# Kernel tuning notes

Hardware: AMD Instinct MI355X
Metric: run time of the kernel (lower is better)

Reference implementation:

```python
import jax, jax.numpy as jnp
import numpy as np

V, E, H, L, B, T = 371, 512, 8, 8, 4, 1024
D = E // H
EPS = 1e-5


def setup_inputs() -> dict:
    key = jax.random.key(0)
    ks = jax.random.split(key, 7)
    s = 0.02
    return {
        "idx": jax.random.randint(ks[0], (B, T), 0, V),
        "wte": jax.random.normal(ks[1], (V, E), jnp.float32) * s,   # tied with lm_head
        "wpe": jax.random.normal(ks[2], (T, E), jnp.float32) * s,
        "c_attn_w": jax.random.normal(ks[3], (L, E, 3 * E), jnp.float32) * s,
        "c_proj_w": jax.random.normal(ks[4], (L, E, E), jnp.float32) * s,
        "fc_w": jax.random.normal(ks[5], (L, E, 4 * E), jnp.float32) * s,
        "fc_proj_w": jax.random.normal(ks[6], (L, 4 * E, E), jnp.float32) * s,
        "ln1_w": jnp.ones((L, E), jnp.float32),
        "ln2_w": jnp.ones((L, E), jnp.float32),
        "lnf_w": jnp.ones((E,), jnp.float32),
    }


def _ln(x, w):
    m = jnp.mean(x, axis=-1, keepdims=True)
    v = jnp.mean((x - m) ** 2, axis=-1, keepdims=True)
    return (x - m) * jax.lax.rsqrt(v + EPS) * w


def reference(idx, wte, wpe, c_attn_w, c_proj_w, fc_w, fc_proj_w, ln1_w, ln2_w, lnf_w):
    mask = jnp.tril(jnp.ones((T, T), bool))  # causal mask, as in the registered buffer
    scale = 1.0 / np.sqrt(D)

    x0 = wte[idx] + wpe[None, :T]  # [B,T,E]

    def block(x, p):
        aw, pw, l1, l2, fw, fpw = p
        h = _ln(x, l1)
        qkv = h @ aw                                   # [B,T,3E]
        q, k, v = jnp.split(qkv, 3, axis=-1)
        q = q.reshape(B, T, H, D)
        k = k.reshape(B, T, H, D)
        v = v.reshape(B, T, H, D)
        att = jnp.einsum("bqhd,bkhd->bhqk", q, k) * scale  # full TxT scores (faithful)
        att = jnp.where(mask[None, None], att, -jnp.inf)
        att = jax.nn.softmax(att, axis=-1)
        y = jnp.einsum("bhqk,bkhd->bqhd", att, v).reshape(B, T, E)
        x = x + y @ pw
        h = _ln(x, l2)
        x = x + jax.nn.gelu(h @ fw, approximate=False) @ fpw
        return x, None

    x, _ = jax.lax.scan(block, x0, (c_attn_w, c_proj_w, ln1_w, ln2_w, fc_w, fc_proj_w))
    x = _ln(x, lnf_w)
    logits = x @ wte.T  # weight tying: lm_head.weight = wte.weight
    return logits
```

## Files before the change

### kernel.cpp

```cpp
#include <hip/hip_runtime.h>


#define VOCAB 371
#define EMB   512
#define NH    8
#define NL    8
#define TS    1024
#define NTOK  4096
#define NEG_INF (-1e30f)

typedef unsigned short ushort_t;
typedef __attribute__((ext_vector_type(8))) short short8;
typedef __attribute__((ext_vector_type(4))) float f32x4;

__device__ inline float bf2f(ushort_t b) {
    unsigned int u = ((unsigned int)b) << 16;
    float f; __builtin_memcpy(&f, &u, 4); return f;
}
__device__ inline ushort_t f2bf(float f) {
    unsigned int u; __builtin_memcpy(&u, &f, 4);
    u = (u + 0x7fff + ((u >> 16) & 1)) >> 16;
    return (ushort_t)u;
}

__global__ __launch_bounds__(64) void detect_k(const ushort_t* __restrict__ w,
        int* __restrict__ flag)
{
    int i = threadIdx.x;
    float v = bf2f(w[2 * i]);
    bool ok = (__builtin_fabsf(v) <= 4.0f);
    unsigned long long m = __ballot(ok);
    if (i == 0) flag[0] = (__popcll(m) >= 56) ? 1 : 0;
}

__global__ __launch_bounds__(256) void sentinel_k(ushort_t* __restrict__ out, int n)
{
    int i = blockIdx.x * 256 + threadIdx.x;
    if (i < n) out[i] = 0x447A;
}

__global__ __launch_bounds__(256) void embed_k(const int* __restrict__ idx,
        const void* __restrict__ wte, const void* __restrict__ wpe,
        float* __restrict__ x, const int* __restrict__ flag)
{
    int n = blockIdx.x, tid = threadIdx.x;
    int t = n & (TS - 1);
    int v = idx[n];
    size_t o = (size_t)n * EMB;
    float a0, a1, b0, b1;
    if (*flag) {
        const ushort_t* te = (const ushort_t*)wte; const ushort_t* pe = (const ushort_t*)wpe;
        a0 = bf2f(te[v * EMB + tid]); a1 = bf2f(te[v * EMB + 256 + tid]);
        b0 = bf2f(pe[t * EMB + tid]); b1 = bf2f(pe[t * EMB + 256 + tid]);
    } else {
        const float* te = (const float*)wte; const float* pe = (const float*)wpe;
        a0 = te[v * EMB + tid]; a1 = te[v * EMB + 256 + tid];
        b0 = pe[t * EMB + tid]; b1 = pe[t * EMB + 256 + tid];
    }
    x[o + tid] = a0 + b0;
    x[o + 256 + tid] = a1 + b1;
}

__global__ __launch_bounds__(256) void ln_k(const float* __restrict__ x,
        const void* __restrict__ w, long woff, ushort_t* __restrict__ out,
        const int* __restrict__ flag)
{
    const int row = blockIdx.x * 4 + (threadIdx.x >> 6);
    const int lane = threadIdx.x & 63;
    const float* xr = x + (size_t)row * EMB + lane * 8;
    float4 f0 = *(const float4*)xr;
    float4 f1 = *(const float4*)(xr + 4);
    float v[8] = {f0.x, f0.y, f0.z, f0.w, f1.x, f1.y, f1.z, f1.w};
    float s = ((v[0] + v[1]) + (v[2] + v[3])) + ((v[4] + v[5]) + (v[6] + v[7]));
#pragma unroll
    for (int off = 32; off > 0; off >>= 1) s += __shfl_xor(s, off, 64);
    float mean = s * (1.0f / EMB);
    float s2 = 0.f;
#pragma unroll
    for (int j = 0; j < 8; ++j) { v[j] -= mean; s2 += v[j] * v[j]; }
#pragma unroll
    for (int off = 32; off > 0; off >>= 1) s2 += __shfl_xor(s2, off, 64);
    float rs = rsqrtf(s2 * (1.0f / EMB) + 1e-5f);
    float g[8];
    if (*flag) {
        const ushort_t* wb = (const ushort_t*)w + woff + lane * 8;
        ushort_t tmp[8];
        *(uint4*)tmp = *(const uint4*)wb;
#pragma unroll
        for (int j = 0; j < 8; ++j) g[j] = bf2f(tmp[j]);
    } else {
        const float* wf = (const float*)w + woff + lane * 8;
        float4 g0 = *(const float4*)wf;
        float4 g1 = *(const float4*)(wf + 4);
        g[0] = g0.x; g[1] = g0.y; g[2] = g0.z; g[3] = g0.w;
        g[4] = g1.x; g[5] = g1.y; g[6] = g1.z; g[7] = g1.w;
    }
    ushort_t ob[8];
#pragma unroll
    for (int j = 0; j < 8; ++j) ob[j] = f2bf(v[j] * rs * g[j]);
    *(uint4*)(out + (size_t)row * EMB + lane * 8) = *(uint4*)ob;
}

__global__ __launch_bounds__(256) void wtrans_k(const void* __restrict__ aw,
        const void* __restrict__ pw, const void* __restrict__ fw,
        const void* __restrict__ fpw, long l, ushort_t* __restrict__ wbuf,
        const int* __restrict__ flag)
{
    __shared__ float tile[64][65];
    const int isbf = *flag;
    long lay = (l < 0) ? (long)blockIdx.z : l;
    ushort_t* obase = wbuf + ((l < 0) ? (size_t)blockIdx.z * 3145728 : 0);
    int t = blockIdx.x;
    const void* src; ushort_t* dst; int Kw, Nw; long ioff;
    if (t < 192)      { src = aw;  dst = obase;           Kw = 512;  Nw = 1536; ioff = lay * 512L * 1536; }
    else if (t < 256) { t -= 192; src = pw;  dst = obase + 786432;  Kw = 512;  Nw = 512;  ioff = lay * 512L * 512; }
    else if (t < 512) { t -= 256; src = fw;  dst = obase + 1048576; Kw = 512;  Nw = 2048; ioff = lay * 512L * 2048; }
    else              { t -= 512; src = fpw; dst = obase + 2097152; Kw = 2048; Nw = 512;  ioff = lay * 2048L * 512; }
    int tn = Nw >> 6;
    int n0 = (t % tn) * 64, k0 = (t / tn) * 64;
    const int r = threadIdx.x >> 2, cq = (threadIdx.x & 3) * 16;
    size_t ii = ioff + (size_t)(k0 + r) * Nw + n0 + cq;
    if (isbf) {
        const ushort_t* sb = (const ushort_t*)src + ii;
        ushort_t tmp[16];
        *(uint4*)tmp = *(const uint4*)sb;
        *(uint4*)(tmp + 8) = *(const uint4*)(sb + 8);
#pragma unroll
        for (int j = 0; j < 16; ++j) tile[r][cq + j] = bf2f(tmp[j]);
    } else {
        const float* sf = (const float*)src + ii;
        *(float4*)&tile[r][cq]      = *(const float4*)sf;
        *(float4*)&tile[r][cq + 4]  = *(const float4*)(sf + 4);
        *(float4*)&tile[r][cq + 8]  = *(const float4*)(sf + 8);
        *(float4*)&tile[r][cq + 12] = *(const float4*)(sf + 12);
    }
    __syncthreads();
    const int kc = (threadIdx.x & 7) * 8;
#pragma unroll
    for (int j = 0; j < 2; ++j) {
        const int n = (threadIdx.x >> 3) + j * 32;
        unsigned pk[4];
#pragma unroll
        for (int i = 0; i < 4; ++i) {
            unsigned lo = f2bf(tile[kc + 2 * i][n]);
            unsigned hi = f2bf(tile[kc + 2 * i + 1][n]);
            pk[i] = lo | (hi << 16);
        }
        *(uint4*)(dst + (size_t)(n0 + n) * Kw + k0 + kc) = *(uint4*)pk;
    }
}

__global__ __launch_bounds__(256) void wconv_k(const void* __restrict__ in,
        ushort_t* __restrict__ out, int n, const int* __restrict__ flag)
{
    int i = blockIdx.x * 256 + threadIdx.x;
    if (i >= n) return;
    out[i] = (*flag) ? ((const ushort_t*)in)[i] : f2bf(((const float*)in)[i]);
}

__global__ __launch_bounds__(256) void gemm_wide(const ushort_t* __restrict__ A,
        const ushort_t* __restrict__ Bt, int M, int N, int K,
        float* __restrict__ outF, ushort_t* __restrict__ outB,
        const float* __restrict__ res, int act)
{
    __shared__ ushort_t Al[128 * 72];
    __shared__ ushort_t Bl[64 * 72];
    const int tid = threadIdx.x;
    const int wave = tid >> 6, lane = tid & 63;
    const int quad = lane >> 4, l16 = lane & 15;
    const int m0 = blockIdx.y * 128, n0 = blockIdx.x * 64;
    const int ar = tid >> 1, ac = (tid & 1) * 32;
    const int br = tid >> 2, bc = (tid & 3) * 16;
    const ushort_t* Ag = A + (size_t)(m0 + ar) * K + ac;
    const ushort_t* Bg = Bt + (size_t)(n0 + br) * K + bc;
    f32x4 acc[2][4] = {};
    for (int k0 = 0; k0 < K; k0 += 64) {
        uint4 a0 = *(const uint4*)(Ag + k0);
        uint4 a1 = *(const uint4*)(Ag + k0 + 8);
        uint4 a2 = *(const uint4*)(Ag + k0 + 16);
        uint4 a3 = *(const uint4*)(Ag + k0 + 24);
        uint4 b0 = *(const uint4*)(Bg + k0);
        uint4 b1 = *(const uint4*)(Bg + k0 + 8);
        __syncthreads();
        *(uint4*)&Al[ar * 72 + ac]      = a0;
        *(uint4*)&Al[ar * 72 + ac + 8]  = a1;
        *(uint4*)&Al[ar * 72 + ac + 16] = a2;
        *(uint4*)&Al[ar * 72 + ac + 24] = a3;
        *(uint4*)&Bl[br * 72 + bc]     = b0;
        *(uint4*)&Bl[br * 72 + bc + 8] = b1;
        __syncthreads();
#pragma unroll
        for (int ks = 0; ks < 2; ++ks) {
            short8 af[2], bf[4];
#pragma unroll
            for (int mi = 0; mi < 2; ++mi)
                af[mi] = *(const short8*)&Al[(wave * 32 + mi * 16 + l16) * 72 + ks * 32 + quad * 8];
#pragma unroll
            for (int ni = 0; ni < 4; ++ni)
                bf[ni] = *(const short8*)&Bl[(ni * 16 + l16) * 72 + ks * 32 + quad * 8];
#pragma unroll
            for (int mi = 0; mi < 2; ++mi)
#pragma unroll
                for (int ni = 0; ni < 4; ++ni)
                    acc[mi][ni] = __builtin_amdgcn_mfma_f32_16x16x32_bf16(
                            af[mi], bf[ni], acc[mi][ni], 0, 0, 0);
        }
    }
#pragma unroll
    for (int mi = 0; mi < 2; ++mi) {
        const int rowb = m0 + wave * 32 + mi * 16 + quad * 4;
#pragma unroll
        for (int ni = 0; ni < 4; ++ni) {
            const int col = n0 + ni * 16 + l16;
#pragma unroll
            for (int r = 0; r < 4; ++r) {
                size_t o = (size_t)(rowb + r) * N + col;
                float v = acc[mi][ni][r];
                if (res) v += res[o];
                if (act) v = 0.5f * v * (1.0f + erff(v * 0.70710678118f));
                if (outF) outF[o] = v;
                else      outB[o] = f2bf(v);
            }
        }
    }
}

__global__ __launch_bounds__(256) void gemm_nt(const ushort_t* __restrict__ A,
        const ushort_t* __restrict__ Bt, int M, int N, int K,
        float* __restrict__ outF, ushort_t* __restrict__ outB, void* __restrict__ outD,
        const float* __restrict__ res, int act, const int* __restrict__ flag)
{
    __shared__ ushort_t Al[64 * 72];
    __shared__ ushort_t Bl[64 * 72];
    const int isbf = *flag;
    const int tid = threadIdx.x;
    const int wave = tid >> 6, lane = tid & 63;
    const int quad = lane >> 4, l16 = lane & 15;
    const int m0 = blockIdx.y * 64, n0 = blockIdx.x * 64;
    const int sr = tid >> 2, sc = (tid & 3) * 16;
    const bool bok = (n0 + sr) < N;
    const ushort_t* Ag = A + (size_t)(m0 + sr) * K + sc;
    const ushort_t* Bg = Bt + (size_t)(n0 + sr) * K + sc;
    f32x4 acc[4] = {};
    for (int k0 = 0; k0 < K; k0 += 64) {
        uint4 a0 = *(const uint4*)(Ag + k0);
        uint4 a1 = *(const uint4*)(Ag + k0 + 8);
        uint4 b0 = make_uint4(0, 0, 0, 0), b1 = make_uint4(0, 0, 0, 0);
        if (bok) { b0 = *(const uint4*)(Bg + k0); b1 = *(const uint4*)(Bg + k0 + 8); }
        __syncthreads();
        *(uint4*)&Al[sr * 72 + sc] = a0; *(uint4*)&Al[sr * 72 + sc + 8] = a1;
        *(uint4*)&Bl[sr * 72 + sc] = b0; *(uint4*)&Bl[sr * 72 + sc + 8] = b1;
        __syncthreads();
#pragma unroll
        for (int kc = 0; kc < 2; ++kc) {
            short8 af = *(const short8*)&Al[(wave * 16 + l16) * 72 + kc * 32 + quad * 8];
#pragma unroll
            for (int nt = 0; nt < 4; ++nt) {
                short8 bf = *(const short8*)&Bl[(nt * 16 + l16) * 72 + kc * 32 + quad * 8];
                acc[nt] = __builtin_amdgcn_mfma_f32_16x16x32_bf16(af, bf, acc[nt], 0, 0, 0);
            }
        }
    }
    const int mb = m0 + wave * 16 + quad * 4;
#pragma unroll
    for (int nt = 0; nt < 4; ++nt) {
        int nn = n0 + nt * 16 + l16;
        if (nn >= N) continue;
#pragma unroll
        for (int r = 0; r < 4; ++r) {
            size_t o = (size_t)(mb + r) * N + nn;
            float v = acc[nt][r];
            if (res) v += res[o];
            if (act) v = 0.5f * v * (1.0f + erff(v * 0.70710678118f));
            if (outF)      outF[o] = v;
            else if (outB) outB[o] = f2bf(v);
            else if (isbf) ((ushort_t*)outD)[o] = f2bf(v);
            else           ((float*)outD)[o] = v;
        }
    }
}

__global__ __launch_bounds__(256) void gemm_k(const ushort_t* __restrict__ A,
        const void* __restrict__ B, long boff, int M, int N, int K, int bt,
        float* __restrict__ outF, ushort_t* __restrict__ outB, void* __restrict__ outD,
        const float* __restrict__ res, int act, const int* __restrict__ flag)
{
    __shared__ ushort_t Al[64 * 40];
    __shared__ ushort_t Bl[64 * 40];
    const int isbf = *flag;
    const int tid = threadIdx.x;
    const int wave = tid >> 6, lane = tid & 63;
    const int quad = lane >> 4, l16 = lane & 15;
    const int m0 = blockIdx.y * 64, n0 = blockIdx.x * 64;
    const int sr = tid >> 2, sc = (tid & 3) * 8;
    const int kr = tid >> 3, nc = (tid & 7) * 8;
    f32x4 acc[4] = {};
    const bool bok = (n0 + sr) < N;
    const ushort_t* Ag = A + (size_t)(m0 + sr) * K + sc;
    const ushort_t* Bb = (const ushort_t*)B + boff;
    const float*    Bf = (const float*)B + boff;
    const size_t i1 = (size_t)(n0 + sr) * K + sc;
    const size_t i0 = (size_t)kr * N + n0 + nc;
    for (int k0 = 0; k0 < K; k0 += 32) {
        uint4 av = *(const uint4*)(Ag + k0);
        ushort_t b8[8] = {0, 0, 0, 0, 0, 0, 0, 0};
        size_t bi = bt ? (i1 + k0) : (i0 + (size_t)k0 * N);
        if (!bt || bok) {
            if (isbf) *(uint4*)b8 = *(const uint4*)(Bb + bi);
            else {
                float4 f0 = *(const float4*)(Bf + bi);
                float4 f1 = *(const float4*)(Bf + bi + 4);
                b8[0] = f2bf(f0.x); b8[1] = f2bf(f0.y); b8[2] = f2bf(f0.z); b8[3] = f2bf(f0.w);
                b8[4] = f2bf(f1.x); b8[5] = f2bf(f1.y); b8[6] = f2bf(f1.z); b8[7] = f2bf(f1.w);
            }
        }
        __syncthreads();
        *(uint4*)&Al[sr * 40 + sc] = av;
        if (bt) *(uint4*)&Bl[sr * 40 + sc] = *(uint4*)b8;
        else {
#pragma unroll
            for (int i = 0; i < 8; ++i) Bl[(nc + i) * 40 + kr] = b8[i];
        }
        __syncthreads();
        short8 af = *(const short8*)&Al[(wave * 16 + l16) * 40 + quad * 8];
#pragma unroll
        for (int nt = 0; nt < 4; ++nt) {
            short8 bf = *(const short8*)&Bl[(nt * 16 + l16) * 40 + quad * 8];
            acc[nt] = __builtin_amdgcn_mfma_f32_16x16x32_bf16(af, bf, acc[nt], 0, 0, 0);
        }
    }
    const int mb = m0 + wave * 16 + quad * 4;
#pragma unroll
    for (int nt = 0; nt < 4; ++nt) {
        int nn = n0 + nt * 16 + l16;
        if (nn >= N) continue;
#pragma unroll
        for (int r = 0; r < 4; ++r) {
            size_t o = (size_t)(mb + r) * N + nn;
            float v = acc[nt][r];
            if (res) v += res[o];
            if (act) v = 0.5f * v * (1.0f + erff(v * 0.70710678118f));
            if (outF)      outF[o] = v;
            else if (outB) outB[o] = f2bf(v);
            else if (isbf) ((ushort_t*)outD)[o] = f2bf(v);
            else           ((float*)outD)[o] = v;
        }
    }
}

__global__ __launch_bounds__(256) void attn_k(const ushort_t* __restrict__ qkv,
        ushort_t* __restrict__ y)
{
    __shared__ ushort_t Kl[64 * 72];
    __shared__ ushort_t Vt[64 * 72];
    __shared__ ushort_t Pl[4][16 * 72];
    const int tid = threadIdx.x, wave = tid >> 6, lane = tid & 63;
    const int quad = lane >> 4, l16 = lane & 15;
    const int qt = (int)gridDim.x - 1 - blockIdx.x;
    const int b = blockIdx.y >> 3, h = blockIdx.y & 7;
    const int q0b = qt * 64;
    const int q0w = q0b + wave * 16;
    const size_t rstr = 3 * EMB;
    const ushort_t* qbase = qkv + ((size_t)(b * TS) + q0w + l16) * rstr + h * 64;
    short8 qf0, qf1;
    {
        ushort_t q0[8], q1[8];
        *(uint4*)q0 = *(const uint4*)(qbase + quad * 8);
        *(uint4*)q1 = *(const uint4*)(qbase + 32 + quad * 8);
#pragma unroll
        for (int i = 0; i < 8; ++i) {
            qf0[i] = (short)f2bf(bf2f(q0[i]) * 0.125f);
            qf1[i] = (short)f2bf(bf2f(q1[i]) * 0.125f);
        }
    }
    short8 onesf;
#pragma unroll
    for (int i = 0; i < 8; ++i) onesf[i] = (short)0x3F80;
    f32x4 O[4] = {};
    f32x4 lacc = {};
    const int sk = tid >> 2, sdc = (tid & 3) * 16;
    const int vp = tid >> 3, vdc = (tid & 7) * 8;
    const int vsh = 16 * ((tid & 7) & 3);
    const int vcol = (2 * vp + vsh) & 63;
    for (int kt = 0; kt <= qt; ++kt) {
        const int k0 = kt * 64;
        const ushort_t* krow = qkv + ((size_t)(b * TS) + k0 + sk) * rstr + EMB + h * 64 + sdc;
        uint4 kv0 = *(const uint4*)krow;
        uint4 kv1 = *(const uint4*)(krow + 8);
        const ushort_t* vrow = qkv + ((size_t)(b * TS) + k0 + 2 * vp) * rstr + 2 * EMB + h * 64 + vdc;
        uint4 vv0 = *(const uint4*)vrow;
        uint4 vv1 = *(const uint4*)(vrow + rstr);
        __syncthreads();
        *(uint4*)&Kl[sk * 72 + sdc]     = kv0;
        *(uint4*)&Kl[sk * 72 + sdc + 8] = kv1;
        {
            ushort_t v0[8], v1[8];
            *(uint4*)v0 = vv0; *(uint4*)v1 = vv1;
#pragma unroll
            for (int i = 0; i < 8; ++i) {
                unsigned pk = (unsigned)v0[i] | ((unsigned)v1[i] << 16);
                *(unsigned*)&Vt[(vdc + i) * 72 + vcol] = pk;
            }
        }
        __syncthreads();
        if (kt < qt) {
            f32x4 S[4] = {};
#pragma unroll
            for (int nt = 0; nt < 4; ++nt) {
                short8 kf0 = *(const short8*)&Kl[(nt * 16 + l16) * 72 + quad * 8];
                short8 kf1 = *(const short8*)&Kl[(nt * 16 + l16) * 72 + 32 + quad * 8];
                S[nt] = __builtin_amdgcn_mfma_f32_16x16x32_bf16(qf0, kf0, S[nt], 0, 0, 0);
                S[nt] = __builtin_amdgcn_mfma_f32_16x16x32_bf16(qf1, kf1, S[nt], 0, 0, 0);
            }
#pragma unroll
            for (int nt = 0; nt < 4; ++nt)
#pragma unroll
                for (int r = 0; r < 4; ++r)
                    Pl[wave][(quad * 4 + r) * 72 + nt * 16 + l16] = f2bf(__expf(S[nt][r]));
        } else {
            f32x4 S[4] = {};
#pragma unroll
            for (int nt = 0; nt < 4; ++nt) {
                if (nt > wave) continue;
                short8 kf0 = *(const short8*)&Kl[(nt * 16 + l16) * 72 + quad * 8];
                short8 kf1 = *(const short8*)&Kl[(nt * 16 + l16) * 72 + 32 + quad * 8];
                S[nt] = __builtin_amdgcn_mfma_f32_16x16x32_bf16(qf0, kf0, S[nt], 0, 0, 0);
                S[nt] = __builtin_amdgcn_mfma_f32_16x16x32_bf16(qf1, kf1, S[nt], 0, 0, 0);
            }
#pragma unroll
            for (int nt = 0; nt < 4; ++nt)
#pragma unroll
                for (int r = 0; r < 4; ++r) {
                    bool live = (nt < wave) || (nt == wave && l16 <= quad * 4 + r);
                    float p = live ? __expf(S[nt][r]) : 0.f;
                    Pl[wave][(quad * 4 + r) * 72 + nt * 16 + l16] = f2bf(p);
                }
        }
#pragma unroll
        for (int kc = 0; kc < 2; ++kc) {
            short8 pf = *(const short8*)&Pl[wave][l16 * 72 + kc * 32 + quad * 8];
            lacc = __builtin_amdgcn_mfma_f32_16x16x32_bf16(pf, onesf, lacc, 0, 0, 0);
#pragma unroll
            for (int dt = 0; dt < 4; ++dt) {
                int d = dt * 16 + l16;
                int sh = ((2 * dt + (l16 >> 3)) & 3) * 16;
                int col = (kc * 32 + quad * 8 + sh) & 63;
                short8 vf = *(const short8*)&Vt[d * 72 + col];
                O[dt] = __builtin_amdgcn_mfma_f32_16x16x32_bf16(pf, vf, O[dt], 0, 0, 0);
            }
        }
    }
#pragma unroll
    for (int dt = 0; dt < 4; ++dt)
#pragma unroll
        for (int r = 0; r < 4; ++r) {
            int q = q0w + quad * 4 + r;
            float v = O[dt][r] / lacc[r];
            y[((size_t)(b * TS) + q) * EMB + h * 64 + dt * 16 + l16] = f2bf(v);
        }
}

extern "C" void kernel_launch(void* const* d_in, const int* in_sizes, int n_in,
                              void* d_out, int out_size, void* d_ws, size_t ws_size,
                              hipStream_t stream)
{
    const int*  idx    = (const int*)d_in[0];
    const void* wte    = d_in[1];
    const void* wpe    = d_in[2];
    const void* attn_w = d_in[3];
    const void* proj_w = d_in[4];
    const void* fc_w   = d_in[5];
    const void* fcp_w  = d_in[6];
    const void* ln1_w  = d_in[7];
    const void* ln2_w  = d_in[8];
    const void* lnf_w  = d_in[9];

    const size_t sz_xw    = (size_t)NTOK * EMB * 4;
    const size_t sz_hbf   = (size_t)NTOK * EMB * 2;
    const size_t sz_big   = (size_t)NTOK * 2048 * 2;
    const size_t sz_wteb  = (size_t)VOCAB * EMB * 2;
    const size_t sz_wbuf1 = (size_t)3145728 * 2;
    const size_t need_legacy = 256 + sz_xw + sz_hbf + sz_big;
    const size_t need_fast   = need_legacy + sz_wteb + sz_wbuf1;
    const size_t need_all    = need_legacy + sz_wteb + NL * sz_wbuf1;

    if (ws_size < need_legacy) {
        sentinel_k<<<(out_size + 255) / 256, 256, 0, stream>>>((ushort_t*)d_out, out_size);
        return;
    }
    int* flag = (int*)d_ws;
    char* p = (char*)d_ws + 256;
    float*    xw  = (float*)p;    p += sz_xw;
    ushort_t* hbf = (ushort_t*)p; p += sz_hbf;
    ushort_t* big = (ushort_t*)p; p += sz_big;

    detect_k<<<1, 64, 0, stream>>>((const ushort_t*)wte, flag);
    embed_k<<<NTOK, 256, 0, stream>>>(idx, wte, wpe, xw, flag);

    if (ws_size >= need_fast) {
        ushort_t* wteb = (ushort_t*)p; p += sz_wteb;
        ushort_t* wbuf = (ushort_t*)p;
        const bool allw = (ws_size >= need_all);
        wconv_k<<<(VOCAB * EMB + 255) / 256, 256, 0, stream>>>(wte, wteb, VOCAB * EMB, flag);
        if (allw)
            wtrans_k<<<dim3(768, 1, NL), 256, 0, stream>>>(attn_w, proj_w, fc_w, fcp_w,
                    -1, wbuf, flag);
        for (int l = 0; l < NL; ++l) {
            ushort_t* wb = allw ? (wbuf + (size_t)l * 3145728) : wbuf;
            if (!allw)
                wtrans_k<<<dim3(768, 1, 1), 256, 0, stream>>>(attn_w, proj_w, fc_w, fcp_w,
                        (long)l, wbuf, flag);
            ln_k<<<NTOK / 4, 256, 0, stream>>>(xw, ln1_w, (long)l * EMB, hbf, flag);
            gemm_wide<<<dim3(24, 32), 256, 0, stream>>>(hbf, wb,
                    NTOK, 1536, 512, nullptr, big, nullptr, 0);
            attn_k<<<dim3(16, 32), 256, 0, stream>>>(big, hbf);
            gemm_nt<<<dim3(8, 64), 256, 0, stream>>>(hbf, wb + 786432,
                    NTOK, 512, 512, xw, nullptr, nullptr, xw, 0, flag);
            ln_k<<<NTOK / 4, 256, 0, stream>>>(xw, ln2_w, (long)l * EMB, hbf, flag);
            gemm_wide<<<dim3(32, 32), 256, 0, stream>>>(hbf, wb + 1048576,
                    NTOK, 2048, 512, nullptr, big, nullptr, 1 );
            gemm_nt<<<dim3(8, 64), 256, 0, stream>>>(big, wb + 2097152,
                    NTOK, 512, 2048, xw, nullptr, nullptr, xw, 0, flag);
        }
        ln_k<<<NTOK / 4, 256, 0, stream>>>(xw, lnf_w, 0, hbf, flag);
        gemm_nt<<<dim3(6, 64), 256, 0, stream>>>(hbf, wteb,
                NTOK, VOCAB, 512, nullptr, nullptr, d_out, nullptr, 0, flag);
    } else {
        for (int l = 0; l < NL; ++l) {
            ln_k<<<NTOK / 4, 256, 0, stream>>>(xw, ln1_w, (long)l * EMB, hbf, flag);
            gemm_k<<<dim3(24, 64), 256, 0, stream>>>(hbf, attn_w, (long)l * 512 * 1536,
                    NTOK, 1536, 512, 0, nullptr, big, nullptr, nullptr, 0, flag);
            attn_k<<<dim3(16, 32), 256, 0, stream>>>(big, hbf);
            gemm_k<<<dim3(8, 64), 256, 0, stream>>>(hbf, proj_w, (long)l * 512 * 512,
                    NTOK, 512, 512, 0, xw, nullptr, nullptr, xw, 0, flag);
            ln_k<<<NTOK / 4, 256, 0, stream>>>(xw, ln2_w, (long)l * EMB, hbf, flag);
            gemm_k<<<dim3(32, 64), 256, 0, stream>>>(hbf, fc_w, (long)l * 512 * 2048,
                    NTOK, 2048, 512, 0, nullptr, big, nullptr, nullptr, 1, flag);
            gemm_k<<<dim3(8, 64), 256, 0, stream>>>(big, fcp_w, (long)l * 2048 * 512,
                    NTOK, 512, 2048, 0, xw, nullptr, nullptr, xw, 0, flag);
        }
        ln_k<<<NTOK / 4, 256, 0, stream>>>(xw, lnf_w, 0, hbf, flag);
        gemm_k<<<dim3(6, 64), 256, 0, stream>>>(hbf, wte, 0,
                NTOK, VOCAB, 512, 1, nullptr, nullptr, d_out, nullptr, 0, flag);
    }
}
```

Before: 1.103 ms.

## Prefetch next K-tile into registers in GEMM and attention loops; pad wte buffer

The GEMM kernels (gemm_wide, gemm_nt) and the attention kernel now load the next K/V tile from global memory into registers right after the LDS stores of the current tile. This lets the global-load latency overlap with the MFMA work on the current tile instead of stalling at the start of each iteration. The converted wte buffer is also padded to 384 rows with zero fill, likely so the lm_head GEMM can read whole tiles without going out of bounds. The prefetch raises register pressure, which may reduce occupancy.

```diff
diff --git a/kernel.cpp b/kernel.cpp
--- a/kernel.cpp
+++ b/kernel.cpp
@@ -2,6 +2,7 @@
 
 
 #define VOCAB 371
+#define VPAD  384
 #define EMB   512
 #define NH    8
 #define NL    8
@@ -151,11 +152,13 @@
 }
 
 __global__ __launch_bounds__(256) void wconv_k(const void* __restrict__ in,
-        ushort_t* __restrict__ out, int n, const int* __restrict__ flag)
+        ushort_t* __restrict__ out, int n, int nreal, const int* __restrict__ flag)
 {
     int i = blockIdx.x * 256 + threadIdx.x;
     if (i >= n) return;
-    out[i] = (*flag) ? ((const ushort_t*)in)[i] : f2bf(((const float*)in)[i]);
+    ushort_t v = 0;
+    if (i < nreal) v = (*flag) ? ((const ushort_t*)in)[i] : f2bf(((const float*)in)[i]);
+    out[i] = v;
 }
 
 __global__ __launch_bounds__(256) void gemm_wide(const ushort_t* __restrict__ A,
@@ -174,13 +177,13 @@
     const ushort_t* Ag = A + (size_t)(m0 + ar) * K + ac;
     const ushort_t* Bg = Bt + (size_t)(n0 + br) * K + bc;
     f32x4 acc[2][4] = {};
+    uint4 a0 = *(const uint4*)(Ag);
+    uint4 a1 = *(const uint4*)(Ag + 8);
+    uint4 a2 = *(const uint4*)(Ag + 16);
+    uint4 a3 = *(const uint4*)(Ag + 24);
+    uint4 b0 = *(const uint4*)(Bg);
+    uint4 b1 = *(const uint4*)(Bg + 8);
     for (int k0 = 0; k0 < K; k0 += 64) {
-        uint4 a0 = *(const uint4*)(Ag + k0);
-        uint4 a1 = *(const uint4*)(Ag + k0 + 8);
-        uint4 a2 = *(const uint4*)(Ag + k0 + 16);
-        uint4 a3 = *(const uint4*)(Ag + k0 + 24);
-        uint4 b0 = *(const uint4*)(Bg + k0);
-        uint4 b1 = *(const uint4*)(Bg + k0 + 8);
         __syncthreads();
         *(uint4*)&Al[ar * 72 + ac]      = a0;
         *(uint4*)&Al[ar * 72 + ac + 8]  = a1;
@@ -189,6 +192,14 @@
         *(uint4*)&Bl[br * 72 + bc]     = b0;
         *(uint4*)&Bl[br * 72 + bc + 8] = b1;
         __syncthreads();
+        if (k0 + 64 < K) {
+            a0 = *(const uint4*)(Ag + k0 + 64);
+            a1 = *(const uint4*)(Ag + k0 + 72);
+            a2 = *(const uint4*)(Ag + k0 + 80);
+            a3 = *(const uint4*)(Ag + k0 + 88);
+            b0 = *(const uint4*)(Bg + k0 + 64);
+            b1 = *(const uint4*)(Bg + k0 + 72);
+        }
 #pragma unroll
         for (int ks = 0; ks < 2; ++ks) {
             short8 af[2], bf[4];
@@ -242,15 +253,23 @@
     const ushort_t* Ag = A + (size_t)(m0 + sr) * K + sc;
     const ushort_t* Bg = Bt + (size_t)(n0 + sr) * K + sc;
     f32x4 acc[4] = {};
+    uint4 a0 = *(const uint4*)(Ag);
+    uint4 a1 = *(const uint4*)(Ag + 8);
+    uint4 b0 = make_uint4(0, 0, 0, 0), b1 = make_uint4(0, 0, 0, 0);
+    if (bok) { b0 = *(const uint4*)(Bg); b1 = *(const uint4*)(Bg + 8); }
     for (int k0 = 0; k0 < K; k0 += 64) {
-        uint4 a0 = *(const uint4*)(Ag + k0);
-        uint4 a1 = *(const uint4*)(Ag + k0 + 8);
-        uint4 b0 = make_uint4(0, 0, 0, 0), b1 = make_uint4(0, 0, 0, 0);
-        if (bok) { b0 = *(const uint4*)(Bg + k0); b1 = *(const uint4*)(Bg + k0 + 8); }
         __syncthreads();
         *(uint4*)&Al[sr * 72 + sc] = a0; *(uint4*)&Al[sr * 72 + sc + 8] = a1;
         *(uint4*)&Bl[sr * 72 + sc] = b0; *(uint4*)&Bl[sr * 72 + sc + 8] = b1;
         __syncthreads();
+        if (k0 + 64 < K) {
+            a0 = *(const uint4*)(Ag + k0 + 64);
+            a1 = *(const uint4*)(Ag + k0 + 72);
+            if (bok) {
+                b0 = *(const uint4*)(Bg + k0 + 64);
+                b1 = *(const uint4*)(Bg + k0 + 72);
+            }
+        }
 #pragma unroll
         for (int kc = 0; kc < 2; ++kc) {
             short8 af = *(const short8*)&Al[(wave * 16 + l16) * 72 + kc * 32 + quad * 8];
@@ -382,14 +401,13 @@
     const int vp = tid >> 3, vdc = (tid & 7) * 8;
     const int vsh = 16 * ((tid & 7) & 3);
     const int vcol = (2 * vp + vsh) & 63;
+    const ushort_t* kbase = qkv + ((size_t)(b * TS) + sk) * rstr + EMB + h * 64 + sdc;
+    const ushort_t* vbase = qkv + ((size_t)(b * TS) + 2 * vp) * rstr + 2 * EMB + h * 64 + vdc;
+    uint4 kv0 = *(const uint4*)(kbase);
+    uint4 kv1 = *(const uint4*)(kbase + 8);
+    uint4 vv0 = *(const uint4*)(vbase);
+    uint4 vv1 = *(const uint4*)(vbase + rstr);
     for (int kt = 0; kt <= qt; ++kt) {
-        const int k0 = kt * 64;
-        const ushort_t* krow = qkv + ((size_t)(b * TS) + k0 + sk) * rstr + EMB + h * 64 + sdc;
-        uint4 kv0 = *(const uint4*)krow;
-        uint4 kv1 = *(const uint4*)(krow + 8);
-        const ushort_t* vrow = qkv + ((size_t)(b * TS) + k0 + 2 * vp) * rstr + 2 * EMB + h * 64 + vdc;
-        uint4 vv0 = *(const uint4*)vrow;
-        uint4 vv1 = *(const uint4*)(vrow + rstr);
         __syncthreads();
         *(uint4*)&Kl[sk * 72 + sdc]     = kv0;
         *(uint4*)&Kl[sk * 72 + sdc + 8] = kv1;
@@ -403,6 +421,13 @@
             }
         }
         __syncthreads();
+        if (kt < qt) {
+            const size_t off = (size_t)(kt + 1) * 64 * rstr;
+            kv0 = *(const uint4*)(kbase + off);
+            kv1 = *(const uint4*)(kbase + off + 8);
+            vv0 = *(const uint4*)(vbase + off);
+            vv1 = *(const uint4*)(vbase + off + rstr);
+        }
         if (kt < qt) {
             f32x4 S[4] = {};
 #pragma unroll
@@ -478,7 +503,7 @@
     const size_t sz_xw    = (size_t)NTOK * EMB * 4;
     const size_t sz_hbf   = (size_t)NTOK * EMB * 2;
     const size_t sz_big   = (size_t)NTOK * 2048 * 2;
-    const size_t sz_wteb  = (size_t)VOCAB * EMB * 2;
+    const size_t sz_wteb  = (size_t)VPAD * EMB * 2;
     const size_t sz_wbuf1 = (size_t)3145728 * 2;
     const size_t need_legacy = 256 + sz_xw + sz_hbf + sz_big;
     const size_t need_fast   = need_legacy + sz_wteb + sz_wbuf1;
@@ -501,7 +526,8 @@
         ushort_t* wteb = (ushort_t*)p; p += sz_wteb;
         ushort_t* wbuf = (ushort_t*)p;
         const bool allw = (ws_size >= need_all);
-        wconv_k<<<(VOCAB * EMB + 255) / 256, 256, 0, stream>>>(wte, wteb, VOCAB * EMB, flag);
+        wconv_k<<<(VPAD * EMB + 255) / 256, 256, 0, stream>>>(wte, wteb,
+                VPAD * EMB, VOCAB * EMB, flag);
         if (allw)
             wtrans_k<<<dim3(768, 1, NL), 256, 0, stream>>>(attn_w, proj_w, fc_w, fcp_w,
                     -1, wbuf, flag);
```

After: 1.109 ms. No clear change (+0.5%).
